# Performance work log

Hardware: AMD Instinct MI355X
Metric: run time of the kernel (lower is better)

## Reference

```python
import jax, jax.numpy as jnp
import numpy as np

VOCAB, EMB_DIM = 50000, 300
HIDDEN, OUT_DIM, N_ASPECTS = 256, 3, 8
BATCH, SEQ = 8192, 128


def setup_inputs() -> dict:
    key = jax.random.key(0)
    k1, k2, k3, k4, k5, k6, k7 = jax.random.split(key, 7)
    input_ids = jax.random.randint(k1, (BATCH, SEQ), 0, VOCAB, dtype=jnp.int64 if jax.config.jax_enable_x64 else jnp.int32)
    aspect_id = jax.random.randint(k2, (BATCH,), 0, N_ASPECTS, dtype=jnp.int32)
    emb = jax.random.normal(k3, (VOCAB, EMB_DIM), dtype=jnp.float32)
    # Per-aspect 2-layer MLP params, stacked along aspect axis. PyTorch Linear
    # init scale ~ U(-1/sqrt(fan_in), 1/sqrt(fan_in)).
    s1 = 1.0 / np.sqrt(EMB_DIM)
    s2 = 1.0 / np.sqrt(HIDDEN)
    W1 = jax.random.uniform(k4, (N_ASPECTS, EMB_DIM, HIDDEN), jnp.float32, -s1, s1)
    b1 = jax.random.uniform(k5, (N_ASPECTS, HIDDEN), jnp.float32, -s1, s1)
    W2 = jax.random.uniform(k6, (N_ASPECTS, HIDDEN, OUT_DIM), jnp.float32, -s2, s2)
    b2 = jax.random.uniform(k7, (N_ASPECTS, OUT_DIM), jnp.float32, -s2, s2)
    return {"input_ids": input_ids, "aspect_id": aspect_id, "emb": emb,
            "W1": W1, "b1": b1, "W2": W2, "b2": b2}


def reference(input_ids, aspect_id, emb, W1, b1, W2, b2):
    # Embedding lookup + mean-pool over sequence -> [B, EMB_DIM]
    x = emb[input_ids].mean(axis=1)
    # Run every sample through every aspect MLP (A is tiny: 8), then select.
    # Same math as per-sample routed MLP, but as A batched GEMMs.
    h = jax.nn.relu(jnp.einsum('bd,adh->abh', x, W1) + b1[:, None, :])  # [A,B,H]
    o = jnp.einsum('abh,aho->abo', h, W2) + b2[:, None, :]              # [A,B,O]
    # Select per-sample expert output: [B, OUT_DIM]
    o_b = jnp.transpose(o, (1, 0, 2))  # [B, A, O]
    return jnp.take_along_axis(o_b, aspect_id[:, None, None], axis=1)[:, 0, :]
```

## Files before the change

kernel.cpp:

```cpp
#include <hip/hip_runtime.h>

constexpr int EMB_DIM   = 300;
constexpr int HIDDEN    = 256;
constexpr int OUT_DIM   = 3;
constexpr int SEQ       = 128;
constexpr int N_ASPECTS = 8;
constexpr int TILE      = 32;
constexpr int MTILE     = 8;

__device__ __forceinline__ unsigned int bfbits(float f) {
  unsigned int u = __float_as_uint(f);
  return (u + 0x7fffu + ((u >> 16) & 1u)) >> 16;
}
__device__ __forceinline__ unsigned int pack2(float lo, float hi) {
  return bfbits(lo) | (bfbits(hi) << 16);
}
__device__ __forceinline__ float blo(unsigned int u) { return __uint_as_float(u << 16); }
__device__ __forceinline__ float bhi(unsigned int u) { return __uint_as_float(u & 0xffff0000u); }

__global__ __launch_bounds__(1024) void prep_kernel(
    const float* __restrict__ emb, unsigned int* __restrict__ emb16, int n8,
    const int* __restrict__ aspect, int B, int* __restrict__ perm, int nperm) {
  const int t = threadIdx.x;

  if (blockIdx.x != 0) {
    int i = (blockIdx.x - 1) * 1024 + t;
    const int stride = (gridDim.x - 1) * 1024;
    for (; i < n8; i += stride) {
      const float4* p = (const float4*)emb + (size_t)i * 2;
      float4 a = p[0], b = p[1];
      uint4 o;
      o.x = pack2(a.x, a.y); o.y = pack2(a.z, a.w);
      o.z = pack2(b.x, b.y); o.w = pack2(b.z, b.w);
      ((uint4*)emb16)[i] = o;
    }
    return;
  }

  const int lane = t & 63, wave = t >> 6;
  __shared__ int wcnt[16][N_ASPECTS];
  __shared__ int cur[16][N_ASPECTS];

  for (int i = t; i < nperm; i += 1024) perm[i] = -1;

  int my_a[8];
  int cnt[N_ASPECTS];
#pragma unroll
  for (int q = 0; q < N_ASPECTS; ++q) cnt[q] = 0;
#pragma unroll
  for (int k = 0; k < 8; ++k) {
    int s = t + k * 1024;
    int a = (s < B) ? aspect[s] : -1;
    my_a[k] = a;
#pragma unroll
    for (int q = 0; q < N_ASPECTS; ++q) cnt[q] += (a == q);
  }
#pragma unroll
  for (int q = 0; q < N_ASPECTS; ++q) {
    int c = cnt[q];
    for (int off = 32; off > 0; off >>= 1) c += __shfl_down(c, off);
    if (lane == 0) wcnt[wave][q] = c;
  }
  __syncthreads();
  if (t == 0) {
    int base = 0;
    for (int q = 0; q < N_ASPECTS; ++q) {
      int tot = 0;
      for (int w = 0; w < 16; ++w) { cur[w][q] = base + tot; tot += wcnt[w][q]; }
      base += ((tot + TILE - 1) / TILE) * TILE;
    }
  }
  __syncthreads();

#pragma unroll
  for (int k = 0; k < 8; ++k) {
    int a = my_a[k];
    int s = t + k * 1024;
#pragma unroll
    for (int q = 0; q < N_ASPECTS; ++q) {
      unsigned long long m = __ballot(a == q);
      if (a == q) {
        int rank = __popcll(m & ((1ull << lane) - 1ull));
        int pos = cur[wave][q] + rank;
        perm[pos] = s;
        if (rank == __popcll(m) - 1) cur[wave][q] = pos + 1;
      }
    }
  }
}

__global__ __launch_bounds__(256) void pool_kernel(
    const int* __restrict__ ids, const unsigned short* __restrict__ emb16,
    float* __restrict__ x, int B) {
  const int wave = threadIdx.x >> 6, lane = threadIdx.x & 63;
  const int b = blockIdx.x * 4 + wave;
  if (b >= B) return;

  int r0 = ids[(size_t)b * SEQ + lane];
  int r1 = ids[(size_t)b * SEQ + lane + 64];

#pragma unroll
  for (int k = 2; k <= 128; k <<= 1) {
#pragma unroll
    for (int j = k >> 1; j >= 1; j >>= 1) {
      if (j == 64) {
        int lo = min(r0, r1), hi = max(r0, r1);
        r0 = lo; r1 = hi;
      } else {
        const bool up0 = ((lane & k) == 0);
        const bool up1 = (((lane + 64) & k) == 0);
        const bool side = ((lane & j) == 0);
        int o0 = __shfl_xor(r0, j);
        int o1 = __shfl_xor(r1, j);
        r0 = (side == up0) ? min(r0, o0) : max(r0, o0);
        r1 = (side == up1) ? min(r1, o1) : max(r1, o1);
      }
    }
  }

  __shared__ int sid[4][SEQ];
  sid[wave][lane]      = r0;
  sid[wave][lane + 64] = r1;
  __syncthreads();

  float a0 = 0.f, a1 = 0.f, a2 = 0.f, a3 = 0.f;
  float c0 = 0.f, c1 = 0.f, c2 = 0.f, c3 = 0.f;
#pragma unroll 4
  for (int s = 0; s < SEQ; ++s) {
    const uint2* __restrict__ r =
        (const uint2*)(emb16 + (size_t)sid[wave][s] * EMB_DIM);
    uint2 v = r[lane];
    a0 += blo(v.x); a1 += bhi(v.x); a2 += blo(v.y); a3 += bhi(v.y);
    if (lane < 11) {
      uint2 w = r[64 + lane];
      c0 += blo(w.x); c1 += bhi(w.x); c2 += blo(w.y); c3 += bhi(w.y);
    }
  }
  const float sc = 1.0f / (float)SEQ;
  float4* __restrict__ xr = (float4*)(x + (size_t)b * EMB_DIM);
  xr[lane] = make_float4(a0 * sc, a1 * sc, a2 * sc, a3 * sc);
  if (lane < 11)
    xr[64 + lane] = make_float4(c0 * sc, c1 * sc, c2 * sc, c3 * sc);
}

__global__ __launch_bounds__(256) void mlp_kernel(
    const float* __restrict__ x, const int* __restrict__ aspect,
    const int* __restrict__ perm,
    const float* __restrict__ W1, const float* __restrict__ b1,
    const float* __restrict__ W2, const float* __restrict__ b2,
    float* __restrict__ out) {
  const int t = threadIdx.x;
  const int wave = t >> 6, lane = t & 63;
  const int g = wave >> 1;
  const int kw = wave & 1;
  const int start = blockIdx.x * MTILE;

  __shared__ int ss[MTILE];
  __shared__ float xch[2][4][64][4];

  if (t < MTILE) ss[t] = perm[start + t];
  __syncthreads();
  const int s0 = ss[0];
  if (s0 < 0) return;
  const int a = aspect[s0];

  int smp[4];
  const float* xrow[4];
#pragma unroll
  for (int s = 0; s < 4; ++s) {
    int m = __builtin_amdgcn_readfirstlane(ss[g * 4 + s]);
    smp[s] = m;
    xrow[s] = x + (size_t)(m < 0 ? s0 : m) * EMB_DIM;
  }

  const float4* __restrict__ w1r =
      (const float4*)(W1 + (size_t)a * EMB_DIM * HIDDEN) + lane;
  float4 acc[4];
  if (kw == 0) {
    const float4 bb = ((const float4*)(b1 + a * HIDDEN))[lane];
#pragma unroll
    for (int s = 0; s < 4; ++s) acc[s] = bb;
  } else {
#pragma unroll
    for (int s = 0; s < 4; ++s) acc[s] = make_float4(0.f, 0.f, 0.f, 0.f);
  }
  const int d0 = kw ? 160 : 0;
  const int d1 = kw ? EMB_DIM : 160;
#pragma unroll 2
  for (int d = d0; d < d1; d += 4) {
    float4 xv[4];
#pragma unroll
    for (int s = 0; s < 4; ++s) xv[s] = *(const float4*)(xrow[s] + d);
#pragma unroll
    for (int dd = 0; dd < 4; ++dd) {
      const float4 w = w1r[(size_t)(d + dd) * (HIDDEN / 4)];
#pragma unroll
      for (int s = 0; s < 4; ++s) {
        const float xs = dd == 0 ? xv[s].x : dd == 1 ? xv[s].y
                        : dd == 2 ? xv[s].z : xv[s].w;
        acc[s].x = fmaf(xs, w.x, acc[s].x);
        acc[s].y = fmaf(xs, w.y, acc[s].y);
        acc[s].z = fmaf(xs, w.z, acc[s].z);
        acc[s].w = fmaf(xs, w.w, acc[s].w);
      }
    }
  }

  if (kw == 0) {
    *(float4*)&xch[g][2][lane][0] = acc[2];
    *(float4*)&xch[g][3][lane][0] = acc[3];
  } else {
    *(float4*)&xch[g][0][lane][0] = acc[0];
    *(float4*)&xch[g][1][lane][0] = acc[1];
  }
  __syncthreads();

  const float4* __restrict__ w2p =
      (const float4*)(W2 + (size_t)a * HIDDEN * OUT_DIM + lane * 12);
  const float4 w2a = w2p[0];
  const float4 w2b = w2p[1];
  const float4 w2c = w2p[2];

  float4 own[2];
  int ms[2];
  if (kw == 0) {
    own[0] = acc[0]; own[1] = acc[1];
    ms[0] = smp[0];  ms[1] = smp[1];
  } else {
    own[0] = acc[2]; own[1] = acc[3];
    ms[0] = smp[2];  ms[1] = smp[3];
  }
  const int mys = 2 * kw;

  float p[2][OUT_DIM];
#pragma unroll
  for (int i = 0; i < 2; ++i) {
    const float4 pr = *(const float4*)&xch[g][mys + i][lane][0];
    const float h0 = fmaxf(own[i].x + pr.x, 0.f);
    const float h1 = fmaxf(own[i].y + pr.y, 0.f);
    const float h2 = fmaxf(own[i].z + pr.z, 0.f);
    const float h3 = fmaxf(own[i].w + pr.w, 0.f);
    p[i][0] = fmaf(h0, w2a.x, fmaf(h1, w2a.w, fmaf(h2, w2b.z, h3 * w2c.y)));
    p[i][1] = fmaf(h0, w2a.y, fmaf(h1, w2b.x, fmaf(h2, w2b.w, h3 * w2c.z)));
    p[i][2] = fmaf(h0, w2a.z, fmaf(h1, w2b.y, fmaf(h2, w2c.x, h3 * w2c.w)));
  }
#pragma unroll
  for (int off = 32; off > 0; off >>= 1)
#pragma unroll
    for (int i = 0; i < 2; ++i) {
      p[i][0] += __shfl_down(p[i][0], off);
      p[i][1] += __shfl_down(p[i][1], off);
      p[i][2] += __shfl_down(p[i][2], off);
    }

  if (lane == 0) {
    const float g0 = b2[a * OUT_DIM + 0];
    const float g1 = b2[a * OUT_DIM + 1];
    const float g2 = b2[a * OUT_DIM + 2];
#pragma unroll
    for (int i = 0; i < 2; ++i) {
      if (ms[i] >= 0) {
        float* o = out + (size_t)ms[i] * OUT_DIM;
        o[0] = p[i][0] + g0;
        o[1] = p[i][1] + g1;
        o[2] = p[i][2] + g2;
      }
    }
  }
}

extern "C" void kernel_launch(void* const* d_in, const int* in_sizes, int n_in,
                              void* d_out, int out_size, void* d_ws, size_t ws_size,
                              hipStream_t stream) {
  const int*   ids    = (const int*)d_in[0];
  const int*   aspect = (const int*)d_in[1];
  const float* emb    = (const float*)d_in[2];
  const float* W1     = (const float*)d_in[3];
  const float* b1     = (const float*)d_in[4];
  const float* W2     = (const float*)d_in[5];
  const float* b2     = (const float*)d_in[6];
  float*       out    = (float*)d_out;

  const int B     = in_sizes[1];
  const int nemb  = in_sizes[2];
  const int nblk  = (B + TILE - 1) / TILE + N_ASPECTS;
  const int nperm = nblk * TILE;

  float* x    = (float*)d_ws;
  int*   perm = (int*)((char*)d_ws + (size_t)B * EMB_DIM * sizeof(float));
  unsigned short* emb16 =
      (unsigned short*)((char*)perm + (((size_t)nperm * 4 + 15) & ~(size_t)15));

  prep_kernel<<<513, 1024, 0, stream>>>(emb, (unsigned int*)emb16, nemb / 8,
                                        aspect, B, perm, nperm);
  pool_kernel<<<(B + 3) / 4, 256, 0, stream>>>(ids, emb16, x, B);
  mlp_kernel<<<nperm / MTILE, 256, 0, stream>>>(x, aspect, perm, W1, b1, W2, b2, out);
}
```

Before: 128.4 us.

## Pad bf16 embedding rows and pool with 16-byte loads and software prefetch

The bf16 embedding copy now stores each vocab row padded to 608 bytes, written one wave per row, so rows are 16-byte aligned. The pooling kernel has each half-wave load a full 512-byte row segment with uint4 loads. It processes four tokens per iteration, spreads the 44-element tail across lanes for several tokens at once, and prefetches the next group's rows into registers. Partial sums are combined with cross-lane shuffles. The aim is fewer, wider, better-aligned gather loads and more memory-level parallelism. The cost is extra padded storage, more registers, and shuffle reductions.

```diff
diff --git a/kernel.cpp b/kernel.cpp
--- a/kernel.cpp
+++ b/kernel.cpp
@@ -7,6 +7,7 @@
 constexpr int N_ASPECTS = 8;
 constexpr int TILE      = 32;
 constexpr int MTILE     = 8;
+constexpr int ROWB      = 608;
 
 __device__ __forceinline__ unsigned int bfbits(float f) {
   unsigned int u = __float_as_uint(f);
@@ -19,25 +20,31 @@
 __device__ __forceinline__ float bhi(unsigned int u) { return __uint_as_float(u & 0xffff0000u); }
 
 __global__ __launch_bounds__(1024) void prep_kernel(
-    const float* __restrict__ emb, unsigned int* __restrict__ emb16, int n8,
+    const float* __restrict__ emb, unsigned short* __restrict__ emb16, int vocab,
     const int* __restrict__ aspect, int B, int* __restrict__ perm, int nperm) {
   const int t = threadIdx.x;
+  const int lane = t & 63, wave = t >> 6;
 
   if (blockIdx.x != 0) {
-    int i = (blockIdx.x - 1) * 1024 + t;
-    const int stride = (gridDim.x - 1) * 1024;
-    for (; i < n8; i += stride) {
-      const float4* p = (const float4*)emb + (size_t)i * 2;
-      float4 a = p[0], b = p[1];
-      uint4 o;
-      o.x = pack2(a.x, a.y); o.y = pack2(a.z, a.w);
-      o.z = pack2(b.x, b.y); o.w = pack2(b.z, b.w);
-      ((uint4*)emb16)[i] = o;
+    const int cw = (blockIdx.x - 1) * 16 + wave;
+    const int nw = (gridDim.x - 1) * 16;
+    for (int v = cw; v < vocab; v += nw) {
+      const float4* __restrict__ src = (const float4*)(emb + (size_t)v * EMB_DIM);
+      char* __restrict__ dst = (char*)emb16 + (size_t)v * ROWB;
+      float4 p = src[lane];
+      uint2 w;
+      w.x = pack2(p.x, p.y); w.y = pack2(p.z, p.w);
+      *(uint2*)(dst + (size_t)lane * 8) = w;
+      if (lane < 11) {
+        float4 q = src[64 + lane];
+        uint2 u;
+        u.x = pack2(q.x, q.y); u.y = pack2(q.z, q.w);
+        *(uint2*)(dst + 512 + (size_t)lane * 8) = u;
+      }
     }
     return;
   }
 
-  const int lane = t & 63, wave = t >> 6;
   __shared__ int wcnt[16][N_ASPECTS];
   __shared__ int cur[16][N_ASPECTS];
 
@@ -118,29 +125,61 @@
     }
   }
 
-  __shared__ int sid[4][SEQ];
-  sid[wave][lane]      = r0;
-  sid[wave][lane + 64] = r1;
-  __syncthreads();
+  __shared__ int sOff[4][SEQ];
+  sOff[wave][lane]      = r0 * ROWB;
+  sOff[wave][lane + 64] = r1 * ROWB;
+
+  const int half = lane >> 5;
+  const int l32  = lane & 31;
+  int myTok = lane / 11, mySub = lane - myTok * 11;
+  if (myTok > 3) { myTok = 3; mySub = 10; }
+  const char* __restrict__ pA = (const char*)emb16 + (size_t)l32 * 16;
+  const char* __restrict__ pB = (const char*)emb16 + 512 + (size_t)mySub * 8;
 
   float a0 = 0.f, a1 = 0.f, a2 = 0.f, a3 = 0.f;
+  float a4 = 0.f, a5 = 0.f, a6 = 0.f, a7 = 0.f;
   float c0 = 0.f, c1 = 0.f, c2 = 0.f, c3 = 0.f;
-#pragma unroll 4
-  for (int s = 0; s < SEQ; ++s) {
-    const uint2* __restrict__ r =
-        (const uint2*)(emb16 + (size_t)sid[wave][s] * EMB_DIM);
-    uint2 v = r[lane];
-    a0 += blo(v.x); a1 += bhi(v.x); a2 += blo(v.y); a3 += bhi(v.y);
-    if (lane < 11) {
-      uint2 w = r[64 + lane];
-      c0 += blo(w.x); c1 += bhi(w.x); c2 += blo(w.y); c3 += bhi(w.y);
-    }
-  }
+
+  uint4 vA0 = *(const uint4*)(pA + sOff[wave][half]);
+  uint4 vA1 = *(const uint4*)(pA + sOff[wave][2 + half]);
+  uint2 vB  = *(const uint2*)(pB + sOff[wave][myTok]);
+
+#pragma unroll 2
+  for (int g = 0; g < 32; ++g) {
+    uint4 nA0, nA1; uint2 nB;
+    if (g < 31) {
+      const int base = 4 * (g + 1);
+      nA0 = *(const uint4*)(pA + sOff[wave][base + half]);
+      nA1 = *(const uint4*)(pA + sOff[wave][base + 2 + half]);
+      nB  = *(const uint2*)(pB + sOff[wave][base + myTok]);
+    }
+    a0 += blo(vA0.x); a1 += bhi(vA0.x); a2 += blo(vA0.y); a3 += bhi(vA0.y);
+    a4 += blo(vA0.z); a5 += bhi(vA0.z); a6 += blo(vA0.w); a7 += bhi(vA0.w);
+    a0 += blo(vA1.x); a1 += bhi(vA1.x); a2 += blo(vA1.y); a3 += bhi(vA1.y);
+    a4 += blo(vA1.z); a5 += bhi(vA1.z); a6 += blo(vA1.w); a7 += bhi(vA1.w);
+    c0 += blo(vB.x);  c1 += bhi(vB.x);  c2 += blo(vB.y);  c3 += bhi(vB.y);
+    vA0 = nA0; vA1 = nA1; vB = nB;
+  }
+
+  a0 += __shfl_down(a0, 32); a1 += __shfl_down(a1, 32);
+  a2 += __shfl_down(a2, 32); a3 += __shfl_down(a3, 32);
+  a4 += __shfl_down(a4, 32); a5 += __shfl_down(a5, 32);
+  a6 += __shfl_down(a6, 32); a7 += __shfl_down(a7, 32);
+  c0 += __shfl_down(c0, 22); c1 += __shfl_down(c1, 22);
+  c2 += __shfl_down(c2, 22); c3 += __shfl_down(c3, 22);
+  c0 += __shfl_down(c0, 11); c1 += __shfl_down(c1, 11);
+  c2 += __shfl_down(c2, 11); c3 += __shfl_down(c3, 11);
+
   const float sc = 1.0f / (float)SEQ;
-  float4* __restrict__ xr = (float4*)(x + (size_t)b * EMB_DIM);
-  xr[lane] = make_float4(a0 * sc, a1 * sc, a2 * sc, a3 * sc);
-  if (lane < 11)
-    xr[64 + lane] = make_float4(c0 * sc, c1 * sc, c2 * sc, c3 * sc);
+  if (lane < 32) {
+    float4* __restrict__ xr = (float4*)(x + (size_t)b * EMB_DIM);
+    xr[lane * 2]     = make_float4(a0 * sc, a1 * sc, a2 * sc, a3 * sc);
+    xr[lane * 2 + 1] = make_float4(a4 * sc, a5 * sc, a6 * sc, a7 * sc);
+  }
+  if (lane < 11) {
+    float4* __restrict__ xb = (float4*)(x + (size_t)b * EMB_DIM + 256);
+    xb[lane] = make_float4(c0 * sc, c1 * sc, c2 * sc, c3 * sc);
+  }
 }
 
 __global__ __launch_bounds__(256) void mlp_kernel(
@@ -283,6 +322,7 @@
 
   const int B     = in_sizes[1];
   const int nemb  = in_sizes[2];
+  const int VOCAB = nemb / EMB_DIM;
   const int nblk  = (B + TILE - 1) / TILE + N_ASPECTS;
   const int nperm = nblk * TILE;
 
@@ -291,7 +331,7 @@
   unsigned short* emb16 =
       (unsigned short*)((char*)perm + (((size_t)nperm * 4 + 15) & ~(size_t)15));
 
-  prep_kernel<<<513, 1024, 0, stream>>>(emb, (unsigned int*)emb16, nemb / 8,
+  prep_kernel<<<513, 1024, 0, stream>>>(emb, emb16, VOCAB,
                                         aspect, B, perm, nperm);
   pool_kernel<<<(B + 3) / 4, 256, 0, stream>>>(ids, emb16, x, B);
   mlp_kernel<<<nperm / MTILE, 256, 0, stream>>>(x, aspect, perm, W1, b1, W2, b2, out);
```

New measurement: 143.1 us. +11.4%, slower.
